# Performance work log

Measured on AMD Instinct MI355X. Metric: run time of the kernel, lower is better.

## Reference

```python
import jax, jax.numpy as jnp
import numpy as np

B, T, N = 128, 20, 49
VOCAB, EMB, HDIM, VDIM, ATT = 10000, 512, 1024, 512, 512
LN_EPS = 1e-5


def _layer_norm(x, g, b):
    mu = x.mean(-1, keepdims=True)
    var = ((x - mu) ** 2).mean(-1, keepdims=True)
    return (x - mu) * jax.lax.rsqrt(var + LN_EPS) * g + b


def _lstm_cell(x, h, c, Wih, Whh, bih, bhh):
    gates = x @ Wih.T + h @ Whh.T + bih + bhh  # [B, 4H]
    i, f, g, o = jnp.split(gates, 4, axis=-1)  # torch LSTMCell gate order
    c_new = jax.nn.sigmoid(f) * c + jax.nn.sigmoid(i) * jnp.tanh(g)
    h_new = jax.nn.sigmoid(o) * jnp.tanh(c_new)
    return h_new, c_new


def setup_inputs() -> dict:
    key = jax.random.key(0)
    ks = jax.random.split(key, 16)
    w = lambda k, shape: (jax.random.normal(k, shape, jnp.float32) * 0.02)
    embed_W = w(ks[2], (VOCAB, EMB)).at[0].set(0.0)  # padding_idx=0 row is zeros
    return dict(
        V=jax.random.normal(ks[0], (B, N, VDIM), jnp.float32),
        y=jax.random.randint(ks[1], (B, T), 0, VOCAB),
        embed_W=embed_W,
        Vp_W=w(ks[3], (HDIM, VDIM)), Vp_b=jnp.zeros((HDIM,), jnp.float32),
        attW=w(ks[4], (ATT, HDIM)), attU=w(ks[5], (ATT, HDIM)), attv=w(ks[6], (1, ATT)),
        l1_Wih=w(ks[7], (4 * HDIM, EMB + HDIM)), l1_Whh=w(ks[8], (4 * HDIM, HDIM)),
        l1_bih=jnp.zeros((4 * HDIM,), jnp.float32), l1_bhh=jnp.zeros((4 * HDIM,), jnp.float32),
        l2_Wih=w(ks[9], (4 * HDIM, HDIM)), l2_Whh=w(ks[10], (4 * HDIM, HDIM)),
        l2_bih=jnp.zeros((4 * HDIM,), jnp.float32), l2_bhh=jnp.zeros((4 * HDIM,), jnp.float32),
        n1_g=jnp.ones((HDIM,), jnp.float32), n1_b=jnp.zeros((HDIM,), jnp.float32),
        n2_g=jnp.ones((HDIM,), jnp.float32), n2_b=jnp.zeros((HDIM,), jnp.float32),
        ih_W=w(ks[11], (HDIM, HDIM)), ih_b=jnp.zeros((HDIM,), jnp.float32),
        ic_W=w(ks[12], (HDIM, HDIM)), ic_b=jnp.zeros((HDIM,), jnp.float32),
        proj_W=w(ks[13], (EMB, HDIM)),
    )


def reference(V, y, embed_W, Vp_W, Vp_b, attW, attU, attv,
              l1_Wih, l1_Whh, l1_bih, l1_bhh,
              l2_Wih, l2_Whh, l2_bih, l2_bhh,
              n1_g, n1_b, n2_g, n2_b,
              ih_W, ih_b, ic_W, ic_b, proj_W):
    Vp = V @ Vp_W.T + Vp_b                      # [B, N, H]
    feat_mean = Vp.mean(1)                      # [B, H]
    h1 = jnp.tanh(feat_mean @ ih_W.T + ih_b)
    c1 = jnp.tanh(feat_mean @ ic_W.T + ic_b)
    h2 = jnp.zeros_like(h1)
    c2 = jnp.zeros_like(c1)

    Uv = Vp @ attU.T                            # [B, N, ATT] (hoisted out of loop)
    emb_y = embed_W[y]                          # [B, T, EMB]
    xs = jnp.swapaxes(emb_y[:, :-1], 0, 1)      # [T-1, B, EMB]

    def step(carry, x_t):
        h1, c1, h2, c2 = carry
        # additive attention (dropout is identity in eval)
        e = jnp.tanh((h2 @ attW.T)[:, None, :] + Uv) @ attv[0]   # [B, N]
        a = jax.nn.softmax(e, axis=1)
        ctx = jnp.einsum('bn,bnh->bh', a, Vp)
        h1n, c1n = _lstm_cell(jnp.concatenate([x_t, ctx], -1), h1, c1,
                              l1_Wih, l1_Whh, l1_bih, l1_bhh)
        h1n = _layer_norm(h1n, n1_g, n1_b)
        h2n, c2n = _lstm_cell(h1n, h2, c2, l2_Wih, l2_Whh, l2_bih, l2_bhh)
        h2n = _layer_norm(h2n, n2_g, n2_b)
        logit = (h2n @ proj_W.T) @ embed_W.T    # [B, VOCAB]
        return (h1n, c1n, h2n, c2n), logit

    _, logits = jax.lax.scan(step, (h1, c1, h2, c2), xs)
    return jnp.swapaxes(logits, 0, 1)           # [B, T-1, VOCAB]
```

## Files before the change

### kernel.cpp

```cpp
#include <hip/hip_runtime.h>
#include <hip/hip_bf16.h>

#define TSTEPS 19

typedef short bf16x8 __attribute__((ext_vector_type(8)));
typedef short bf16x4 __attribute__((ext_vector_type(4)));
typedef float f32x4 __attribute__((ext_vector_type(4)));

__device__ __forceinline__ f32x4 mfma_bf16(bf16x8 a, bf16x8 b, f32x4 c) {
    return __builtin_amdgcn_mfma_f32_16x16x32_bf16(a, b, c, 0, 0, 0);
}
__device__ __forceinline__ short f2b(float f) {
    union { float f; unsigned u; } v; v.f = f;
    unsigned r = v.u + 0x7fffu + ((v.u >> 16) & 1u);
    return (short)(r >> 16);
}
__device__ __forceinline__ float b2f(short s) {
    union { unsigned u; float f; } v; v.u = ((unsigned)(unsigned short)s) << 16;
    return v.f;
}
__device__ __forceinline__ float sigm(float x) { return 1.f / (1.f + __expf(-x)); }
__device__ __forceinline__ float tanhfast(float x) { return 1.f - 2.f / (__expf(2.f * x) + 1.f); }

__global__ __launch_bounds__(256) void k_convert(
    const float* __restrict__ l1_Wih, const float* __restrict__ l1_Whh,
    const float* __restrict__ l2_Wih, const float* __restrict__ l2_Whh,
    const float* __restrict__ embed_W, const float* __restrict__ proj_W,
    const float* __restrict__ attW, const float* __restrict__ ih_W,
    const float* __restrict__ ic_W, const float* __restrict__ Vp_W,
    const float* __restrict__ attU, const float* __restrict__ V,
    const int* __restrict__ y, const float* __restrict__ n1g,
    const float* __restrict__ n2g,
    short* __restrict__ l1h, short* __restrict__ l1l,
    short* __restrict__ l2h, short* __restrict__ l2l,
    short* __restrict__ embB, short* __restrict__ pa, short* __restrict__ ihic,
    short* __restrict__ VpWh, short* __restrict__ VpWl, short* __restrict__ attUb,
    short* __restrict__ Vbh, short* __restrict__ Vbl, short* __restrict__ xall) {
    const int N1 = 4096 * 2560, N2 = 4096 * 2048, N3 = 10000 * 512, N4 = 1024 * 1024,
              N5 = 2048 * 1024, N6 = 1024 * 512, N7 = 512 * 1024, N8 = 128 * 49 * 512,
              N9 = 19 * 128 * 512;
    const int total4 = (N1 + N2 + N3 + N4 + N5 + N6 + N7 + N8 + N9) >> 2;
    int stride = gridDim.x * blockDim.x;
    for (int g = blockIdx.x * blockDim.x + threadIdx.x; g < total4; g += stride) {
        int e = g << 2;
        if (e < N1) {
            int n = e / 2560, k = e - n * 2560;
            f32x4 v;
            if (k < 1536) {
                v = *(const f32x4*)(l1_Wih + (size_t)n * 1536 + k);
            } else {
                f32x4 w = *(const f32x4*)(l1_Whh + (size_t)n * 1024 + (k - 1536));
                f32x4 gg = *(const f32x4*)(n1g + (k - 1536));
#pragma unroll
                for (int j = 0; j < 4; j++) v[j] = gg[j] * w[j];
            }
            bf16x4 hi, lo;
#pragma unroll
            for (int j = 0; j < 4; j++) { hi[j] = f2b(v[j]); lo[j] = f2b(v[j] - b2f(hi[j])); }
            *(bf16x4*)(l1h + e) = hi; *(bf16x4*)(l1l + e) = lo; continue;
        }
        e -= N1;
        if (e < N2) {
            int n = e >> 11, k = e & 2047;
            f32x4 w, gg;
            if (k < 1024) {
                w = *(const f32x4*)(l2_Wih + (size_t)n * 1024 + k);
                gg = *(const f32x4*)(n1g + k);
            } else {
                w = *(const f32x4*)(l2_Whh + (size_t)n * 1024 + (k - 1024));
                gg = *(const f32x4*)(n2g + (k - 1024));
            }
            bf16x4 hi, lo;
#pragma unroll
            for (int j = 0; j < 4; j++) {
                float v = gg[j] * w[j];
                hi[j] = f2b(v); lo[j] = f2b(v - b2f(hi[j]));
            }
            *(bf16x4*)(l2h + e) = hi; *(bf16x4*)(l2l + e) = lo; continue;
        }
        e -= N2;
        if (e < N3) {
            f32x4 v = *(const f32x4*)(embed_W + e);
            bf16x4 o;
#pragma unroll
            for (int j = 0; j < 4; j++) o[j] = f2b(v[j]);
            *(bf16x4*)(embB + e) = o; continue;
        }
        e -= N3;
        if (e < N4) {
            int n = e >> 10, k = e & 1023;
            f32x4 w = (n < 512) ? *(const f32x4*)(proj_W + (size_t)n * 1024 + k)
                                : *(const f32x4*)(attW + (size_t)(n - 512) * 1024 + k);
            f32x4 gg = *(const f32x4*)(n2g + k);
            bf16x4 o;
#pragma unroll
            for (int j = 0; j < 4; j++) o[j] = f2b(gg[j] * w[j]);
            *(bf16x4*)(pa + e) = o; continue;
        }
        e -= N4;
        if (e < N5) {
            int n = e >> 10, k = e & 1023;
            f32x4 w = (n < 1024) ? *(const f32x4*)(ih_W + (size_t)n * 1024 + k)
                                 : *(const f32x4*)(ic_W + (size_t)(n - 1024) * 1024 + k);
            bf16x4 o;
#pragma unroll
            for (int j = 0; j < 4; j++) o[j] = f2b(w[j]);
            *(bf16x4*)(ihic + e) = o; continue;
        }
        e -= N5;
        if (e < N6) {
            f32x4 v = *(const f32x4*)(Vp_W + e);
            bf16x4 hi, lo;
#pragma unroll
            for (int j = 0; j < 4; j++) { hi[j] = f2b(v[j]); lo[j] = f2b(v[j] - b2f(hi[j])); }
            *(bf16x4*)(VpWh + e) = hi; *(bf16x4*)(VpWl + e) = lo; continue;
        }
        e -= N6;
        if (e < N7) {
            f32x4 v = *(const f32x4*)(attU + e);
            bf16x4 o;
#pragma unroll
            for (int j = 0; j < 4; j++) o[j] = f2b(v[j]);
            *(bf16x4*)(attUb + e) = o; continue;
        }
        e -= N7;
        if (e < N8) {
            f32x4 v = *(const f32x4*)(V + e);
            bf16x4 hi, lo;
#pragma unroll
            for (int j = 0; j < 4; j++) { hi[j] = f2b(v[j]); lo[j] = f2b(v[j] - b2f(hi[j])); }
            *(bf16x4*)(Vbh + e) = hi; *(bf16x4*)(Vbl + e) = lo; continue;
        }
        e -= N8;
        {
            int t = e >> 16; int r = e & 65535;
            int b = r >> 9, k = r & 511;
            int idx = y[b * 20 + t];
            f32x4 v = *(const f32x4*)(embed_W + (size_t)idx * 512 + k);
            bf16x4 o;
#pragma unroll
            for (int j = 0; j < 4; j++) o[j] = f2b(v[j]);
            *(bf16x4*)(xall + e) = o;
        }
    }
}

__global__ __launch_bounds__(256) void k_corr(
    const float* __restrict__ l1_Whh, const float* __restrict__ l2_Wih,
    const float* __restrict__ l2_Whh, const float* __restrict__ proj_W,
    const float* __restrict__ attW,
    const float* __restrict__ n1g, const float* __restrict__ n1b,
    const float* __restrict__ n2g, const float* __restrict__ n2b,
    float* __restrict__ wg1, float* __restrict__ wb1,
    float* __restrict__ wg2a, float* __restrict__ wb2a,
    float* __restrict__ wg2b, float* __restrict__ wb2b,
    float* __restrict__ wgp, float* __restrict__ wbp) {
    int w = (blockIdx.x * 256 + threadIdx.x) >> 6;
    int lane = threadIdx.x & 63;
    if (w >= 13312) return;
    const float* row; const float* g; const float* b; float* og; float* ob;
    if (w < 4096)       { row = l1_Whh + (size_t)w * 1024; g = n1g; b = n1b; og = wg1 + w; ob = wb1 + w; }
    else if (w < 8192)  { int j = w - 4096; row = l2_Wih + (size_t)j * 1024; g = n1g; b = n1b; og = wg2a + j; ob = wb2a + j; }
    else if (w < 12288) { int j = w - 8192; row = l2_Whh + (size_t)j * 1024; g = n2g; b = n2b; og = wg2b + j; ob = wb2b + j; }
    else                { int j = w - 12288;
                          row = (j < 512) ? proj_W + (size_t)j * 1024 : attW + (size_t)(j - 512) * 1024;
                          g = n2g; b = n2b; og = wgp + j; ob = wbp + j; }
    float sg = 0.f, sb = 0.f;
    for (int k = lane; k < 1024; k += 64) { float wv = row[k]; sg += g[k] * wv; sb += b[k] * wv; }
#pragma unroll
    for (int o = 1; o < 64; o <<= 1) { sg += __shfl_xor(sg, o); sb += __shfl_xor(sb, o); }
    if (lane == 0) { *og = sg; *ob = sb; }
}

__device__ __forceinline__ void gemm_core(const short* __restrict__ A, int lda,
                                          const short* __restrict__ Bm, int ldb,
                                          int mb, int n0, int K, int Nlim,
                                          f32x4 acc[2][4]) {
    int lane = threadIdx.x & 63, wave = threadIdx.x >> 6;
    int col = lane & 15, quad = lane >> 4;
    const short* a0p = A + (size_t)(mb + wave * 32 + col) * lda + quad * 8;
    const short* a1p = a0p + (size_t)16 * lda;
    const short* bp[4];
#pragma unroll
    for (int s = 0; s < 4; s++) {
        int n = n0 + s * 16 + col;
        if (n >= Nlim) n = 0;
        bp[s] = Bm + (size_t)n * ldb + quad * 8;
    }
    for (int kb = 0; kb < K; kb += 32) {
        bf16x8 a0 = *(const bf16x8*)(a0p + kb);
        bf16x8 a1 = *(const bf16x8*)(a1p + kb);
#pragma unroll
        for (int s = 0; s < 4; s++) {
            bf16x8 b = *(const bf16x8*)(bp[s] + kb);
            acc[0][s] = mfma_bf16(a0, b, acc[0][s]);
            acc[1][s] = mfma_bf16(a1, b, acc[1][s]);
        }
    }
}

__global__ __launch_bounds__(256) void k_gemm_vp(const short* __restrict__ Ah,
                                                 const short* __restrict__ Al,
                                                 const short* __restrict__ Bh,
                                                 const short* __restrict__ Bl,
                                                 const float* __restrict__ Vp_b,
                                                 short* __restrict__ Vph,
                                                 short* __restrict__ Vpl) {
    int lane = threadIdx.x & 63, wave = threadIdx.x >> 6, col = lane & 15, quad = lane >> 4;
    int mb = blockIdx.y * 128, n0 = blockIdx.x * 64;
    f32x4 acc[2][4] = {};
    const short* ah0 = Ah + (size_t)(mb + wave * 32 + col) * 512 + quad * 8;
    const short* al0 = Al + (size_t)(mb + wave * 32 + col) * 512 + quad * 8;
    const short* ah1 = ah0 + 16 * 512; const short* al1 = al0 + 16 * 512;
    const short* bh[4]; const short* bl[4];
#pragma unroll
    for (int s = 0; s < 4; s++) {
        int n = n0 + s * 16 + col;
        bh[s] = Bh + (size_t)n * 512 + quad * 8; bl[s] = Bl + (size_t)n * 512 + quad * 8;
    }
    for (int kb = 0; kb < 512; kb += 32) {
        bf16x8 h0 = *(const bf16x8*)(ah0 + kb), l0 = *(const bf16x8*)(al0 + kb);
        bf16x8 h1 = *(const bf16x8*)(ah1 + kb), l1 = *(const bf16x8*)(al1 + kb);
#pragma unroll
        for (int s = 0; s < 4; s++) {
            bf16x8 wh = *(const bf16x8*)(bh[s] + kb);
            bf16x8 wl = *(const bf16x8*)(bl[s] + kb);
            acc[0][s] = mfma_bf16(h0, wh, acc[0][s]);
            acc[0][s] = mfma_bf16(l0, wh, acc[0][s]);
            acc[0][s] = mfma_bf16(h0, wl, acc[0][s]);
            acc[1][s] = mfma_bf16(h1, wh, acc[1][s]);
            acc[1][s] = mfma_bf16(l1, wh, acc[1][s]);
            acc[1][s] = mfma_bf16(h1, wl, acc[1][s]);
        }
    }
#pragma unroll
    for (int i = 0; i < 2; i++)
#pragma unroll
        for (int s = 0; s < 4; s++) {
            int n = n0 + s * 16 + col;
            float bias = Vp_b[n];
#pragma unroll
            for (int r = 0; r < 4; r++) {
                int m = mb + wave * 32 + i * 16 + quad * 4 + r;
                float v = acc[i][s][r] + bias;
                short hi = f2b(v);
                Vph[(size_t)m * 1024 + n] = hi;
                Vpl[(size_t)m * 1024 + n] = f2b(v - b2f(hi));
            }
        }
}

__global__ __launch_bounds__(256) void k_gemm_uv(const short* __restrict__ Vph,
                                                 const short* __restrict__ Vpl,
                                                 const short* __restrict__ attUb,
                                                 short* __restrict__ Uv) {
    int lane = threadIdx.x & 63, wave = threadIdx.x >> 6, col = lane & 15, quad = lane >> 4;
    int mb = blockIdx.y * 128, n0 = blockIdx.x * 64;
    f32x4 acc[2][4] = {};
    const short* ah0 = Vph + (size_t)(mb + wave * 32 + col) * 1024 + quad * 8;
    const short* al0 = Vpl + (size_t)(mb + wave * 32 + col) * 1024 + quad * 8;
    const short* ah1 = ah0 + 16 * 1024; const short* al1 = al0 + 16 * 1024;
    const short* bp[4];
#pragma unroll
    for (int s = 0; s < 4; s++) bp[s] = attUb + (size_t)(n0 + s * 16 + col) * 1024 + quad * 8;
    for (int kb = 0; kb < 1024; kb += 32) {
        bf16x8 h0 = *(const bf16x8*)(ah0 + kb), l0 = *(const bf16x8*)(al0 + kb);
        bf16x8 h1 = *(const bf16x8*)(ah1 + kb), l1 = *(const bf16x8*)(al1 + kb);
#pragma unroll
        for (int s = 0; s < 4; s++) {
            bf16x8 b = *(const bf16x8*)(bp[s] + kb);
            acc[0][s] = mfma_bf16(h0, b, acc[0][s]);
            acc[0][s] = mfma_bf16(l0, b, acc[0][s]);
            acc[1][s] = mfma_bf16(h1, b, acc[1][s]);
            acc[1][s] = mfma_bf16(l1, b, acc[1][s]);
        }
    }
#pragma unroll
    for (int i = 0; i < 2; i++)
#pragma unroll
        for (int s = 0; s < 4; s++) {
            int n = n0 + s * 16 + col;
#pragma unroll
            for (int r = 0; r < 4; r++) {
                int m = mb + wave * 32 + i * 16 + quad * 4 + r;
                Uv[(size_t)m * 512 + n] = f2b(acc[i][s][r]);
            }
        }
}

__global__ __launch_bounds__(256) void k_gemm_xpart(const short* __restrict__ xall,
                                                    const short* __restrict__ l1h,
                                                    float* __restrict__ xpart) {
    f32x4 acc[2][4] = {};
    int mb = blockIdx.y * 128, n0 = blockIdx.x * 64;
    gemm_core(xall, 512, l1h, 2560, mb, n0, 512, 1 << 30, acc);
    int lane = threadIdx.x & 63, wave = threadIdx.x >> 6, col = lane & 15, quad = lane >> 4;
#pragma unroll
    for (int i = 0; i < 2; i++)
#pragma unroll
        for (int s = 0; s < 4; s++) {
            int n = n0 + s * 16 + col;
#pragma unroll
            for (int r = 0; r < 4; r++) {
                int m = mb + wave * 32 + i * 16 + quad * 4 + r;
                xpart[(size_t)m * 4096 + n] = acc[i][s][r];
            }
        }
}

__global__ __launch_bounds__(256) void k_feat(const short* __restrict__ Vph,
                                              const short* __restrict__ Vpl,
                                              short* __restrict__ feat,
                                              float* __restrict__ c2,
                                              short* __restrict__ h2h1,
                                              short* __restrict__ h2l1,
                                              float* __restrict__ st1,
                                              float* __restrict__ st2) {
    int b = blockIdx.x, tid = threadIdx.x;
    int h0 = tid * 4;
    float acc[4] = {0.f, 0.f, 0.f, 0.f};
    for (int n = 0; n < 49; n++) {
        bf16x4 vh = *(const bf16x4*)(Vph + ((size_t)b * 49 + n) * 1024 + h0);
        bf16x4 vl = *(const bf16x4*)(Vpl + ((size_t)b * 49 + n) * 1024 + h0);
#pragma unroll
        for (int j = 0; j < 4; j++) acc[j] += b2f(vh[j]) + b2f(vl[j]);
    }
    bf16x4 o;
#pragma unroll
    for (int j = 0; j < 4; j++) o[j] = f2b(acc[j] * (1.f / 49.f));
    *(bf16x4*)(feat + (size_t)b * 1024 + h0) = o;
#pragma unroll
    for (int j = 0; j < 4; j++) {
        c2[(size_t)b * 1024 + h0 + j] = 0.f;
        h2h1[(size_t)b * 1024 + h0 + j] = 0;
        h2l1[(size_t)b * 1024 + h0 + j] = 0;
    }
    if (tid == 0) {
        st1[(128 + b) * 2] = 0.f; st1[(128 + b) * 2 + 1] = 1.f;
        st2[(128 + b) * 2] = 0.f; st2[(128 + b) * 2 + 1] = 1.f;
    }
}

__global__ __launch_bounds__(256) void k_gemm_h1c1(const short* __restrict__ feat,
                                                   const short* __restrict__ ihic,
                                                   const float* __restrict__ ih_b,
                                                   const float* __restrict__ ic_b,
                                                   short* __restrict__ h1h1,
                                                   short* __restrict__ h1l1,
                                                   float* __restrict__ c1) {
    f32x4 acc[2][4] = {};
    int n0 = blockIdx.y * 64;
    gemm_core(feat, 1024, ihic, 1024, 0, n0, 1024, 1 << 30, acc);
    int lane = threadIdx.x & 63, wave = threadIdx.x >> 6, col = lane & 15, quad = lane >> 4;
#pragma unroll
    for (int i = 0; i < 2; i++)
#pragma unroll
        for (int s = 0; s < 4; s++) {
            int n = n0 + s * 16 + col;
#pragma unroll
            for (int r = 0; r < 4; r++) {
                int m = wave * 32 + i * 16 + quad * 4 + r;
                float v = acc[i][s][r];
                if (n < 1024) {
                    float t = tanhfast(v + ih_b[n]);
                    short hi = f2b(t);
                    h1h1[(size_t)m * 1024 + n] = hi;
                    h1l1[(size_t)m * 1024 + n] = f2b(t - b2f(hi));
                } else {
                    c1[(size_t)m * 1024 + (n - 1024)] = tanhfast(v + ic_b[n - 1024]);
                }
            }
        }
}

__global__ __launch_bounds__(256) void k_attn(
        int t,
        const float* __restrict__ pproj,
        const float* __restrict__ st2p,
        const float* __restrict__ wgp, const float* __restrict__ wbp,
        short* __restrict__ pbuf_prev,
        const short* __restrict__ Uv,
        const float* __restrict__ attv, const short* __restrict__ Vph,
        const short* __restrict__ Vpl,
        short* __restrict__ ctxh, short* __restrict__ ctxl) {
    int b = blockIdx.x, tid = threadIdx.x;
    int lane = tid & 63, wave = tid >> 6;
    __shared__ float shW[512];
    __shared__ float se[49], sa[49];
    if (t == 0) {
        shW[tid] = 0.f; shW[tid + 256] = 0.f;
    } else {
        float mu = st2p[b * 2], rs = st2p[b * 2 + 1];
        int n4 = tid * 4;
        f32x4 p0 = *(const f32x4*)(pproj + (size_t)b * 1024 + n4);
        f32x4 p1 = *(const f32x4*)(pproj + 131072 + (size_t)b * 1024 + n4);
        f32x4 wb = *(const f32x4*)(wbp + n4);
        f32x4 wg = *(const f32x4*)(wgp + n4);
        float v[4];
#pragma unroll
        for (int j = 0; j < 4; j++) v[j] = rs * (p0[j] + p1[j]) + wb[j] - rs * mu * wg[j];
        if (n4 < 512) {
            bf16x4 o;
#pragma unroll
            for (int j = 0; j < 4; j++) o[j] = f2b(v[j]);
            *(bf16x4*)(pbuf_prev + (size_t)b * 512 + n4) = o;
        } else {
#pragma unroll
            for (int j = 0; j < 4; j++) shW[n4 - 512 + j] = v[j];
        }
    }
    __syncthreads();
    for (int n = wave; n < 49; n += 4) {
        const float* hw = shW + lane * 8;
        const short* uv = Uv + ((size_t)b * 49 + n) * 512 + lane * 8;
        const float* av = attv + lane * 8;
        bf16x8 u8 = *(const bf16x8*)uv;
        float part = 0.f;
#pragma unroll
        for (int j = 0; j < 8; j++) part += tanhfast(hw[j] + b2f(u8[j])) * av[j];
#pragma unroll
        for (int o = 1; o < 64; o <<= 1) part += __shfl_xor(part, o);
        if (lane == 0) se[n] = part;
    }
    __syncthreads();
    if (wave == 0) {
        float v = (lane < 49) ? se[lane] : -1e30f;
        float mx = v;
#pragma unroll
        for (int o = 1; o < 64; o <<= 1) mx = fmaxf(mx, __shfl_xor(mx, o));
        float p = (lane < 49) ? __expf(v - mx) : 0.f;
        float s = p;
#pragma unroll
        for (int o = 1; o < 64; o <<= 1) s += __shfl_xor(s, o);
        if (lane < 49) sa[lane] = p / s;
    }
    __syncthreads();
    {
        int h0 = tid * 4;
        float acc[4] = {0.f, 0.f, 0.f, 0.f};
        for (int n = 0; n < 49; n++) {
            float wgt = sa[n];
            bf16x4 vh = *(const bf16x4*)(Vph + ((size_t)b * 49 + n) * 1024 + h0);
            bf16x4 vl = *(const bf16x4*)(Vpl + ((size_t)b * 49 + n) * 1024 + h0);
#pragma unroll
            for (int j = 0; j < 4; j++) acc[j] += wgt * (b2f(vh[j]) + b2f(vl[j]));
        }
        bf16x4 oh, ol;
#pragma unroll
        for (int j = 0; j < 4; j++) {
            short hi = f2b(acc[j]); oh[j] = hi; ol[j] = f2b(acc[j] - b2f(hi));
        }
        *(bf16x4*)(ctxh + (size_t)b * 1024 + h0) = oh;
        *(bf16x4*)(ctxl + (size_t)b * 1024 + h0) = ol;
    }
}

__global__ __launch_bounds__(256) void k_lstm1_mm(
        const short* __restrict__ ctxh, const short* __restrict__ ctxl,
        const short* __restrict__ h1hp, const short* __restrict__ h1lp,
        const short* __restrict__ l1h, const short* __restrict__ l1l,
        float* __restrict__ part) {
    int bn = blockIdx.x, bk = blockIdx.y;
    int lane = threadIdx.x & 63, wave = threadIdx.x >> 6, col = lane & 15, quad = lane >> 4;
    int n0 = bn * 64;
    int kw0 = 512 + bk * 512;
    f32x4 acc[2][4] = {};
    const short* bh[4]; const short* bl[4];
#pragma unroll
    for (int s = 0; s < 4; s++) {
        size_t o = (size_t)(n0 + s * 16 + col) * 2560 + kw0 + quad * 8;
        bh[s] = l1h + o; bl[s] = l1l + o;
    }
    int r0 = wave * 32 + col;
    const short* Ah = (bk < 2) ? ctxh : h1hp;
    const short* Al = (bk < 2) ? ctxl : h1lp;
    int ko = (bk & 1) * 512;
    const short* a0h = Ah + (size_t)r0 * 1024 + ko + quad * 8;
    const short* a0l = Al + (size_t)r0 * 1024 + ko + quad * 8;
    const short* a1h = a0h + 16 * 1024; const short* a1l = a0l + 16 * 1024;
    for (int kb = 0; kb < 512; kb += 32) {
        bf16x8 h0 = *(const bf16x8*)(a0h + kb), l0 = *(const bf16x8*)(a0l + kb);
        bf16x8 h1 = *(const bf16x8*)(a1h + kb), l1 = *(const bf16x8*)(a1l + kb);
#pragma unroll
        for (int s = 0; s < 4; s++) {
            bf16x8 wh = *(const bf16x8*)(bh[s] + kb);
            bf16x8 wl = *(const bf16x8*)(bl[s] + kb);
            acc[0][s] = mfma_bf16(h0, wh, acc[0][s]);
            acc[0][s] = mfma_bf16(l0, wh, acc[0][s]);
            acc[0][s] = mfma_bf16(h0, wl, acc[0][s]);
            acc[1][s] = mfma_bf16(h1, wh, acc[1][s]);
            acc[1][s] = mfma_bf16(l1, wh, acc[1][s]);
            acc[1][s] = mfma_bf16(h1, wl, acc[1][s]);
        }
    }
#pragma unroll
    for (int i = 0; i < 2; i++)
#pragma unroll
        for (int s = 0; s < 4; s++)
#pragma unroll
            for (int r = 0; r < 4; r++) {
                int m = wave * 32 + i * 16 + quad * 4 + r;
                part[((size_t)bk * 128 + m) * 4096 + n0 + s * 16 + col] = acc[i][s][r];
            }
}

__global__ __launch_bounds__(256) void k_red1(const float* __restrict__ part,
        const float* __restrict__ xpart_t,
        const float* __restrict__ st_prev,
        const float* __restrict__ wg1, const float* __restrict__ wb1,
        const float* __restrict__ bih, const float* __restrict__ bhh,
        float* __restrict__ c1, short* __restrict__ h1hc, short* __restrict__ h1lc,
        float* __restrict__ st_cur) {
    int m = blockIdx.x, tid = threadIdx.x;
    float mu_p = st_prev[m * 2], rs_p = st_prev[m * 2 + 1];
    const size_t SB = 128UL * 4096;
    int h = tid * 4;
    float pre[4][4];
#pragma unroll
    for (int g = 0; g < 4; g++) {
        int n = g * 1024 + h;
        size_t base = (size_t)m * 4096 + n;
        f32x4 pX = *(const f32x4*)(xpart_t + base);
        f32x4 p0 = *(const f32x4*)(part + base);
        f32x4 p1 = *(const f32x4*)(part + SB + base);
        f32x4 p2 = *(const f32x4*)(part + 2 * SB + base);
        f32x4 p3 = *(const f32x4*)(part + 3 * SB + base);
        f32x4 wb = *(const f32x4*)(wb1 + n);
        f32x4 wg = *(const f32x4*)(wg1 + n);
        f32x4 bi = *(const f32x4*)(bih + n);
        f32x4 bh = *(const f32x4*)(bhh + n);
#pragma unroll
        for (int j = 0; j < 4; j++)
            pre[g][j] = (pX[j] + p0[j] + p1[j]) + rs_p * (p2[j] + p3[j])
                        + wb[j] - rs_p * mu_p * wg[j] + bi[j] + bh[j];
    }
    size_t idx = (size_t)m * 1024 + h;
    f32x4 cv = *(const f32x4*)(c1 + idx);
    f32x4 cn_v; bf16x4 oh, ol;
    float s1 = 0.f, s2 = 0.f;
#pragma unroll
    for (int j = 0; j < 4; j++) {
        float cn = sigm(pre[1][j]) * cv[j] + sigm(pre[0][j]) * tanhfast(pre[2][j]);
        float hn = sigm(pre[3][j]) * tanhfast(cn);
        cn_v[j] = cn;
        short hi = f2b(hn); oh[j] = hi; ol[j] = f2b(hn - b2f(hi));
        s1 += hn; s2 += hn * hn;
    }
    *(f32x4*)(c1 + idx) = cn_v;
    *(bf16x4*)(h1hc + idx) = oh;
    *(bf16x4*)(h1lc + idx) = ol;
    __shared__ float red[8];
    int lane = tid & 63, wave = tid >> 6;
#pragma unroll
    for (int o = 1; o < 64; o <<= 1) { s1 += __shfl_xor(s1, o); s2 += __shfl_xor(s2, o); }
    if (lane == 0) { red[wave * 2] = s1; red[wave * 2 + 1] = s2; }
    __syncthreads();
    if (tid == 0) {
        float S1 = red[0] + red[2] + red[4] + red[6];
        float S2 = red[1] + red[3] + red[5] + red[7];
        float mu = S1 * (1.f / 1024.f);
        float var = S2 * (1.f / 1024.f) - mu * mu;
        st_cur[m * 2] = mu; st_cur[m * 2 + 1] = rsqrtf(var + 1e-5f);
    }
}

__global__ __launch_bounds__(256) void k_lstm2_mm(
        const short* __restrict__ h1hc, const short* __restrict__ h1lc,
        const short* __restrict__ h2hp, const short* __restrict__ h2lp,
        const short* __restrict__ l2h, const short* __restrict__ l2l,
        float* __restrict__ part) {
    int bn = blockIdx.x, bk = blockIdx.y;
    int lane = threadIdx.x & 63, wave = threadIdx.x >> 6, col = lane & 15, quad = lane >> 4;
    int n0 = bn * 64;
    int kw0 = bk * 512;
    f32x4 acc[2][4] = {};
    const short* bh[4]; const short* bl[4];
#pragma unroll
    for (int s = 0; s < 4; s++) {
        size_t o = (size_t)(n0 + s * 16 + col) * 2048 + kw0 + quad * 8;
        bh[s] = l2h + o; bl[s] = l2l + o;
    }
    int r0 = wave * 32 + col;
    const short* Ah = (bk < 2) ? h1hc : h2hp;
    const short* Al = (bk < 2) ? h1lc : h2lp;
    int ko = (bk & 1) * 512;
    const short* a0h = Ah + (size_t)r0 * 1024 + ko + quad * 8;
    const short* a0l = Al + (size_t)r0 * 1024 + ko + quad * 8;
    const short* a1h = a0h + 16 * 1024; const short* a1l = a0l + 16 * 1024;
    for (int kb = 0; kb < 512; kb += 32) {
        bf16x8 h0 = *(const bf16x8*)(a0h + kb), l0 = *(const bf16x8*)(a0l + kb);
        bf16x8 h1 = *(const bf16x8*)(a1h + kb), l1 = *(const bf16x8*)(a1l + kb);
#pragma unroll
        for (int s = 0; s < 4; s++) {
            bf16x8 wh = *(const bf16x8*)(bh[s] + kb);
            bf16x8 wl = *(const bf16x8*)(bl[s] + kb);
            acc[0][s] = mfma_bf16(h0, wh, acc[0][s]);
            acc[0][s] = mfma_bf16(l0, wh, acc[0][s]);
            acc[0][s] = mfma_bf16(h0, wl, acc[0][s]);
            acc[1][s] = mfma_bf16(h1, wh, acc[1][s]);
            acc[1][s] = mfma_bf16(l1, wh, acc[1][s]);
            acc[1][s] = mfma_bf16(h1, wl, acc[1][s]);
        }
    }
#pragma unroll
    for (int i = 0; i < 2; i++)
#pragma unroll
        for (int s = 0; s < 4; s++)
#pragma unroll
            for (int r = 0; r < 4; r++) {
                int m = wave * 32 + i * 16 + quad * 4 + r;
                part[((size_t)bk * 128 + m) * 4096 + n0 + s * 16 + col] = acc[i][s][r];
            }
}

__global__ __launch_bounds__(256) void k_red2(const float* __restrict__ part,
        const float* __restrict__ stA, const float* __restrict__ stB,
        const float* __restrict__ wg2a, const float* __restrict__ wb2a,
        const float* __restrict__ wg2b, const float* __restrict__ wb2b,
        const float* __restrict__ bih, const float* __restrict__ bhh,
        float* __restrict__ c2, short* __restrict__ h2hc, short* __restrict__ h2lc,
        float* __restrict__ st_cur) {
    int m = blockIdx.x, tid = threadIdx.x;
    float mu1 = stA[m * 2], rs1 = stA[m * 2 + 1];
    float mu2 = stB[m * 2], rs2 = stB[m * 2 + 1];
    const size_t SB = 128UL * 4096;
    int h = tid * 4;
    float pre[4][4];
#pragma unroll
    for (int g = 0; g < 4; g++) {
        int n = g * 1024 + h;
        size_t base = (size_t)m * 4096 + n;
        f32x4 p0 = *(const f32x4*)(part + base);
        f32x4 p1 = *(const f32x4*)(part + SB + base);
        f32x4 p2 = *(const f32x4*)(part + 2 * SB + base);
        f32x4 p3 = *(const f32x4*)(part + 3 * SB + base);
        f32x4 wba = *(const f32x4*)(wb2a + n);
        f32x4 wga = *(const f32x4*)(wg2a + n);
        f32x4 wbb = *(const f32x4*)(wb2b + n);
        f32x4 wgb = *(const f32x4*)(wg2b + n);
        f32x4 bi = *(const f32x4*)(bih + n);
        f32x4 bh = *(const f32x4*)(bhh + n);
#pragma unroll
        for (int j = 0; j < 4; j++)
            pre[g][j] = rs1 * (p0[j] + p1[j]) + rs2 * (p2[j] + p3[j])
                        + wba[j] - rs1 * mu1 * wga[j]
                        + wbb[j] - rs2 * mu2 * wgb[j] + bi[j] + bh[j];
    }
    size_t idx = (size_t)m * 1024 + h;
    f32x4 cv = *(const f32x4*)(c2 + idx);
    f32x4 cn_v; bf16x4 oh, ol;
    float s1 = 0.f, s2 = 0.f;
#pragma unroll
    for (int j = 0; j < 4; j++) {
        float cn = sigm(pre[1][j]) * cv[j] + sigm(pre[0][j]) * tanhfast(pre[2][j]);
        float hn = sigm(pre[3][j]) * tanhfast(cn);
        cn_v[j] = cn;
        short hi = f2b(hn); oh[j] = hi; ol[j] = f2b(hn - b2f(hi));
        s1 += hn; s2 += hn * hn;
    }
    *(f32x4*)(c2 + idx) = cn_v;
    *(bf16x4*)(h2hc + idx) = oh;
    *(bf16x4*)(h2lc + idx) = ol;
    __shared__ float red[8];
    int lane = tid & 63, wave = tid >> 6;
#pragma unroll
    for (int o = 1; o < 64; o <<= 1) { s1 += __shfl_xor(s1, o); s2 += __shfl_xor(s2, o); }
    if (lane == 0) { red[wave * 2] = s1; red[wave * 2 + 1] = s2; }
    __syncthreads();
    if (tid == 0) {
        float S1 = red[0] + red[2] + red[4] + red[6];
        float S2 = red[1] + red[3] + red[5] + red[7];
        float mu = S1 * (1.f / 1024.f);
        float var = S2 * (1.f / 1024.f) - mu * mu;
        st_cur[m * 2] = mu; st_cur[m * 2 + 1] = rsqrtf(var + 1e-5f);
    }
}

__global__ __launch_bounds__(256) void k_projatt(
        const short* __restrict__ h2hc, const short* __restrict__ h2lc,
        const short* __restrict__ pa,
        float* __restrict__ pproj) {
    int nt = blockIdx.x, mh = blockIdx.y, kc = blockIdx.z;
    int tid = threadIdx.x, lane = tid & 63, wave = tid >> 6, col = lane & 15, quad = lane >> 4;
    int arow = mh * 64 + wave * 16 + col;
    int n = nt * 16 + col;
    int k0 = kc * 512;
    f32x4 acc = {};
    const short* bp = pa + (size_t)n * 1024 + k0 + quad * 8;
    const short* ah = h2hc + (size_t)arow * 1024 + k0 + quad * 8;
    const short* al = h2lc + (size_t)arow * 1024 + k0 + quad * 8;
    for (int kb = 0; kb < 512; kb += 32) {
        bf16x8 xh = *(const bf16x8*)(ah + kb);
        bf16x8 xl = *(const bf16x8*)(al + kb);
        bf16x8 b = *(const bf16x8*)(bp + kb);
        acc = mfma_bf16(xh, b, acc);
        acc = mfma_bf16(xl, b, acc);
    }
#pragma unroll
    for (int r = 0; r < 4; r++) {
        int m = mh * 64 + wave * 16 + quad * 4 + r;
        pproj[(size_t)kc * 131072 + (size_t)m * 1024 + nt * 16 + col] = acc[r];
    }
}

__global__ __launch_bounds__(256) void k_pbuf(const float* __restrict__ pproj,
        const float* __restrict__ st2c,
        const float* __restrict__ wgp, const float* __restrict__ wbp,
        short* __restrict__ pbuf) {
    int b = blockIdx.x, tid = threadIdx.x;
    float mu = st2c[b * 2], rs = st2c[b * 2 + 1];
#pragma unroll
    for (int j = 0; j < 2; j++) {
        int n = tid * 2 + j;
        float v = rs * (pproj[(size_t)b * 1024 + n] + pproj[131072 + (size_t)b * 1024 + n])
                  + wbp[n] - rs * mu * wgp[n];
        pbuf[(size_t)b * 512 + n] = f2b(v);
    }
}

__global__ __launch_bounds__(256) void k_logits_all(const short* __restrict__ pbuf_all,
                                                    const short* __restrict__ embB,
                                                    float* __restrict__ out) {
    int n0 = blockIdx.x * 64, t = blockIdx.y;
    __shared__ alignas(16) short Bs[64 * 512];
    char* Bsb = (char*)Bs;
    int tid = threadIdx.x, lane = tid & 63, wave = tid >> 6;
#pragma unroll
    for (int i = 0; i < 16; i++) {
        int r = i * 4 + wave;
        int n = n0 + r; if (n >= 10000) n = 0;
        bf16x8 v = *(const bf16x8*)(embB + (size_t)n * 512 + lane * 8);
        *(bf16x8*)(Bsb + r * 1024 + ((lane * 16) ^ ((r & 7) << 4))) = v;
    }
    __syncthreads();
    int col = lane & 15, quad = lane >> 4;
    f32x4 acc[2][4] = {};
    const short* A = pbuf_all + (size_t)t * 128 * 512;
    const short* a0p = A + (size_t)(wave * 32 + col) * 512 + quad * 8;
    const short* a1p = a0p + 16 * 512;
    int rbase[4], rkey[4];
#pragma unroll
    for (int s = 0; s < 4; s++) {
        int r = s * 16 + col;
        rbase[s] = r * 1024;
        rkey[s] = (r & 7) << 4;
    }
#pragma unroll 4
    for (int kb = 0; kb < 512; kb += 32) {
        bf16x8 a0 = *(const bf16x8*)(a0p + kb);
        bf16x8 a1 = *(const bf16x8*)(a1p + kb);
#pragma unroll
        for (int s = 0; s < 4; s++) {
            bf16x8 bfrag = *(const bf16x8*)(Bsb + rbase[s] + ((quad * 16 + kb * 2) ^ rkey[s]));
            acc[0][s] = mfma_bf16(a0, bfrag, acc[0][s]);
            acc[1][s] = mfma_bf16(a1, bfrag, acc[1][s]);
        }
    }
#pragma unroll
    for (int i = 0; i < 2; i++)
#pragma unroll
        for (int s = 0; s < 4; s++) {
            int n = n0 + s * 16 + col;
            if (n >= 10000) continue;
#pragma unroll
            for (int r = 0; r < 4; r++) {
                int m = wave * 32 + i * 16 + quad * 4 + r;
                out[((size_t)m * 19 + t) * 10000 + n] = acc[i][s][r];
            }
        }
}

extern "C" void kernel_launch(void* const* d_in, const int* in_sizes, int n_in,
                              void* d_out, int out_size, void* d_ws, size_t ws_size,
                              hipStream_t stream) {
    const float* V = (const float*)d_in[0];
    const int* y = (const int*)d_in[1];
    const float* embed_W = (const float*)d_in[2];
    const float* Vp_W = (const float*)d_in[3];
    const float* Vp_b = (const float*)d_in[4];
    const float* attW = (const float*)d_in[5];
    const float* attU = (const float*)d_in[6];
    const float* attv = (const float*)d_in[7];
    const float* l1_Wih = (const float*)d_in[8];
    const float* l1_Whh = (const float*)d_in[9];
    const float* l1_bih = (const float*)d_in[10];
    const float* l1_bhh = (const float*)d_in[11];
    const float* l2_Wih = (const float*)d_in[12];
    const float* l2_Whh = (const float*)d_in[13];
    const float* l2_bih = (const float*)d_in[14];
    const float* l2_bhh = (const float*)d_in[15];
    const float* n1g = (const float*)d_in[16];
    const float* n1b = (const float*)d_in[17];
    const float* n2g = (const float*)d_in[18];
    const float* n2b = (const float*)d_in[19];
    const float* ih_W = (const float*)d_in[20];
    const float* ih_b = (const float*)d_in[21];
    const float* ic_W = (const float*)d_in[22];
    const float* ic_b = (const float*)d_in[23];
    const float* proj_W = (const float*)d_in[24];
    float* out = (float*)d_out;
    (void)in_sizes; (void)n_in; (void)out_size;

    char* wsp = (char*)d_ws;
    size_t off = 0;
    auto alloc = [&](size_t bytes) -> void* {
        void* p = wsp + off;
        off += (bytes + 255) & ~(size_t)255;
        return p;
    };
    short* l1h  = (short*)alloc(4096UL * 2560 * 2);
    short* l1l  = (short*)alloc(4096UL * 2560 * 2);
    short* l2h  = (short*)alloc(4096UL * 2048 * 2);
    short* l2l  = (short*)alloc(4096UL * 2048 * 2);
    short* embB = (short*)alloc(10000UL * 512 * 2);
    short* pa   = (short*)alloc(1024UL * 1024 * 2);
    short* ihic = (short*)alloc(2048UL * 1024 * 2);
    short* VpWh = (short*)alloc(1024UL * 512 * 2);
    short* VpWl = (short*)alloc(1024UL * 512 * 2);
    short* attUb= (short*)alloc(512UL * 1024 * 2);
    short* Vbh  = (short*)alloc(128UL * 49 * 512 * 2);
    short* Vbl  = (short*)alloc(128UL * 49 * 512 * 2);
    short* xall = (short*)alloc(19UL * 128 * 512 * 2);
    short* Vph  = (short*)alloc(6272UL * 1024 * 2);
    short* Vpl  = (short*)alloc(6272UL * 1024 * 2);
    short* Uv   = (short*)alloc(6272UL * 512 * 2);
    short* feat = (short*)alloc(128UL * 1024 * 2);
    short* ctxh = (short*)alloc(128UL * 1024 * 2);
    short* ctxl = (short*)alloc(128UL * 1024 * 2);
    short* h1h  = (short*)alloc(2UL * 128 * 1024 * 2);
    short* h1l  = (short*)alloc(2UL * 128 * 1024 * 2);
    short* h2h  = (short*)alloc(2UL * 128 * 1024 * 2);
    short* h2l  = (short*)alloc(2UL * 128 * 1024 * 2);
    short* pbuf_all = (short*)alloc(19UL * 128 * 512 * 2);
    float* c1   = (float*)alloc(128UL * 1024 * 4);
    float* c2   = (float*)alloc(128UL * 1024 * 4);
    float* st1  = (float*)alloc(2UL * 128 * 2 * 4);
    float* st2  = (float*)alloc(2UL * 128 * 2 * 4);
    float* pmm1 = (float*)alloc(4UL * 128 * 4096 * 4);
    float* pmm2 = (float*)alloc(4UL * 128 * 4096 * 4);
    float* pproj= (float*)alloc(2UL * 128 * 1024 * 4);
    float* xpart= (float*)alloc(2432UL * 4096 * 4);
    float* wg1  = (float*)alloc(4096UL * 4);
    float* wb1  = (float*)alloc(4096UL * 4);
    float* wg2a = (float*)alloc(4096UL * 4);
    float* wb2a = (float*)alloc(4096UL * 4);
    float* wg2b = (float*)alloc(4096UL * 4);
    float* wb2b = (float*)alloc(4096UL * 4);
    float* wgp  = (float*)alloc(1024UL * 4);
    float* wbp  = (float*)alloc(1024UL * 4);
    if (off > ws_size) return;

    const size_t HB = 128UL * 1024;
    const size_t SB2 = 128UL * 2;

    k_convert<<<2048, 256, 0, stream>>>(l1_Wih, l1_Whh, l2_Wih, l2_Whh, embed_W, proj_W,
                                        attW, ih_W, ic_W, Vp_W, attU, V, y, n1g, n2g,
                                        l1h, l1l, l2h, l2l, embB, pa, ihic,
                                        VpWh, VpWl, attUb, Vbh, Vbl, xall);
    k_corr<<<3328, 256, 0, stream>>>(l1_Whh, l2_Wih, l2_Whh, proj_W, attW,
                                     n1g, n1b, n2g, n2b,
                                     wg1, wb1, wg2a, wb2a, wg2b, wb2b, wgp, wbp);
    k_gemm_vp<<<dim3(16, 49), 256, 0, stream>>>(Vbh, Vbl, VpWh, VpWl, Vp_b, Vph, Vpl);
    k_gemm_xpart<<<dim3(64, 19), 256, 0, stream>>>(xall, l1h, xpart);
    k_feat<<<128, 256, 0, stream>>>(Vph, Vpl, feat, c2, h2h + HB, h2l + HB, st1, st2);
    k_gemm_h1c1<<<dim3(1, 32), 256, 0, stream>>>(feat, ihic, ih_b, ic_b,
                                                 h1h + HB, h1l + HB, c1);
    k_gemm_uv<<<dim3(8, 49), 256, 0, stream>>>(Vph, Vpl, attUb, Uv);

    for (int t = 0; t < TSTEPS; t++) {
        int cur = t & 1, prev = cur ^ 1;
        short* pbuf_prev = pbuf_all + (size_t)(t > 0 ? t - 1 : 0) * 128 * 512;
        k_attn<<<128, 256, 0, stream>>>(t, pproj, st2 + prev * SB2, wgp, wbp,
                                        pbuf_prev, Uv, attv, Vph, Vpl, ctxh, ctxl);
        k_lstm1_mm<<<dim3(64, 4), 256, 0, stream>>>(ctxh, ctxl,
                                                    h1h + prev * HB, h1l + prev * HB,
                                                    l1h, l1l, pmm1);
        k_red1<<<128, 256, 0, stream>>>(pmm1, xpart + (size_t)t * 128 * 4096,
                                        st1 + prev * SB2, wg1, wb1,
                                        l1_bih, l1_bhh, c1,
                                        h1h + cur * HB, h1l + cur * HB, st1 + cur * SB2);
        k_lstm2_mm<<<dim3(64, 4), 256, 0, stream>>>(h1h + cur * HB, h1l + cur * HB,
                                                    h2h + prev * HB, h2l + prev * HB,
                                                    l2h, l2l, pmm2);
        k_red2<<<128, 256, 0, stream>>>(pmm2, st1 + cur * SB2, st2 + prev * SB2,
                                        wg2a, wb2a, wg2b, wb2b, l2_bih, l2_bhh, c2,
                                        h2h + cur * HB, h2l + cur * HB, st2 + cur * SB2);
        k_projatt<<<dim3(64, 2, 2), 256, 0, stream>>>(h2h + cur * HB, h2l + cur * HB,
                                                      pa, pproj);
    }
    k_pbuf<<<128, 256, 0, stream>>>(pproj, st2, wgp, wbp,
                                    pbuf_all + 18UL * 128 * 512);
    k_logits_all<<<dim3(157, 19), 256, 0, stream>>>(pbuf_all, embB, out);
}
```

Before: 2.332 ms.

## Stage weight tiles in swizzled LDS and double split-K for LSTM GEMMs

The Vp, Uv and both per-step LSTM GEMM kernels now copy each block's weight tile into shared memory once, using an XOR swizzle. Previously every wave read the shared B operand straight from global memory. The LSTM matmuls split K eight ways instead of four, giving 512 blocks per launch for more parallelism, and the reduce kernels sum eight partial buffers. The two partial buffers are merged into one. In exchange there are extra syncs, 64KB of LDS per block that limits occupancy, and more partial-sum traffic in the reductions.

```diff
diff --git a/kernel.cpp b/kernel.cpp
--- a/kernel.cpp
+++ b/kernel.cpp
@@ -206,31 +206,46 @@
                                                  const float* __restrict__ Vp_b,
                                                  short* __restrict__ Vph,
                                                  short* __restrict__ Vpl) {
-    int lane = threadIdx.x & 63, wave = threadIdx.x >> 6, col = lane & 15, quad = lane >> 4;
+    __shared__ alignas(16) short Bs[2 * 64 * 256];
+    char* Bsb = (char*)Bs;
+    int tid = threadIdx.x, lane = tid & 63, wave = tid >> 6, col = lane & 15, quad = lane >> 4;
     int mb = blockIdx.y * 128, n0 = blockIdx.x * 64;
     f32x4 acc[2][4] = {};
     const short* ah0 = Ah + (size_t)(mb + wave * 32 + col) * 512 + quad * 8;
     const short* al0 = Al + (size_t)(mb + wave * 32 + col) * 512 + quad * 8;
     const short* ah1 = ah0 + 16 * 512; const short* al1 = al0 + 16 * 512;
-    const short* bh[4]; const short* bl[4];
-#pragma unroll
-    for (int s = 0; s < 4; s++) {
-        int n = n0 + s * 16 + col;
-        bh[s] = Bh + (size_t)n * 512 + quad * 8; bl[s] = Bl + (size_t)n * 512 + quad * 8;
-    }
-    for (int kb = 0; kb < 512; kb += 32) {
-        bf16x8 h0 = *(const bf16x8*)(ah0 + kb), l0 = *(const bf16x8*)(al0 + kb);
-        bf16x8 h1 = *(const bf16x8*)(ah1 + kb), l1 = *(const bf16x8*)(al1 + kb);
-#pragma unroll
-        for (int s = 0; s < 4; s++) {
-            bf16x8 wh = *(const bf16x8*)(bh[s] + kb);
-            bf16x8 wl = *(const bf16x8*)(bl[s] + kb);
-            acc[0][s] = mfma_bf16(h0, wh, acc[0][s]);
-            acc[0][s] = mfma_bf16(l0, wh, acc[0][s]);
-            acc[0][s] = mfma_bf16(h0, wl, acc[0][s]);
-            acc[1][s] = mfma_bf16(h1, wh, acc[1][s]);
-            acc[1][s] = mfma_bf16(l1, wh, acc[1][s]);
-            acc[1][s] = mfma_bf16(h1, wl, acc[1][s]);
+#pragma unroll
+    for (int ph = 0; ph < 2; ph++) {
+        int kbase = ph * 256;
+        __syncthreads();
+#pragma unroll
+        for (int i = 0; i < 8; i++) {
+            int r = i * 8 + wave * 2 + (lane >> 5);
+            int n = n0 + r;
+            int e = (lane & 31) * 8;
+            bf16x8 vh = *(const bf16x8*)(Bh + (size_t)n * 512 + kbase + e);
+            bf16x8 vl = *(const bf16x8*)(Bl + (size_t)n * 512 + kbase + e);
+            int wo = r * 512 + ((e * 2) ^ ((r & 7) << 4));
+            *(bf16x8*)(Bsb + wo) = vh;
+            *(bf16x8*)(Bsb + 32768 + wo) = vl;
+        }
+        __syncthreads();
+        for (int kb = 0; kb < 256; kb += 32) {
+            bf16x8 h0 = *(const bf16x8*)(ah0 + kbase + kb), l0 = *(const bf16x8*)(al0 + kbase + kb);
+            bf16x8 h1 = *(const bf16x8*)(ah1 + kbase + kb), l1 = *(const bf16x8*)(al1 + kbase + kb);
+#pragma unroll
+            for (int s = 0; s < 4; s++) {
+                int r = s * 16 + col;
+                int off = r * 512 + ((quad * 16 + kb * 2) ^ ((r & 7) << 4));
+                bf16x8 wh = *(const bf16x8*)(Bsb + off);
+                bf16x8 wl = *(const bf16x8*)(Bsb + 32768 + off);
+                acc[0][s] = mfma_bf16(h0, wh, acc[0][s]);
+                acc[0][s] = mfma_bf16(l0, wh, acc[0][s]);
+                acc[0][s] = mfma_bf16(h0, wl, acc[0][s]);
+                acc[1][s] = mfma_bf16(h1, wh, acc[1][s]);
+                acc[1][s] = mfma_bf16(l1, wh, acc[1][s]);
+                acc[1][s] = mfma_bf16(h1, wl, acc[1][s]);
+            }
         }
     }
 #pragma unroll
@@ -254,25 +269,39 @@
                                                  const short* __restrict__ Vpl,
                                                  const short* __restrict__ attUb,
                                                  short* __restrict__ Uv) {
-    int lane = threadIdx.x & 63, wave = threadIdx.x >> 6, col = lane & 15, quad = lane >> 4;
+    __shared__ alignas(16) short Bs[64 * 512];
+    char* Bsb = (char*)Bs;
+    int tid = threadIdx.x, lane = tid & 63, wave = tid >> 6, col = lane & 15, quad = lane >> 4;
     int mb = blockIdx.y * 128, n0 = blockIdx.x * 64;
     f32x4 acc[2][4] = {};
     const short* ah0 = Vph + (size_t)(mb + wave * 32 + col) * 1024 + quad * 8;
     const short* al0 = Vpl + (size_t)(mb + wave * 32 + col) * 1024 + quad * 8;
     const short* ah1 = ah0 + 16 * 1024; const short* al1 = al0 + 16 * 1024;
-    const short* bp[4];
-#pragma unroll
-    for (int s = 0; s < 4; s++) bp[s] = attUb + (size_t)(n0 + s * 16 + col) * 1024 + quad * 8;
-    for (int kb = 0; kb < 1024; kb += 32) {
-        bf16x8 h0 = *(const bf16x8*)(ah0 + kb), l0 = *(const bf16x8*)(al0 + kb);
-        bf16x8 h1 = *(const bf16x8*)(ah1 + kb), l1 = *(const bf16x8*)(al1 + kb);
-#pragma unroll
-        for (int s = 0; s < 4; s++) {
-            bf16x8 b = *(const bf16x8*)(bp[s] + kb);
-            acc[0][s] = mfma_bf16(h0, b, acc[0][s]);
-            acc[0][s] = mfma_bf16(l0, b, acc[0][s]);
-            acc[1][s] = mfma_bf16(h1, b, acc[1][s]);
-            acc[1][s] = mfma_bf16(l1, b, acc[1][s]);
+#pragma unroll
+    for (int ph = 0; ph < 2; ph++) {
+        int kbase = ph * 512;
+        __syncthreads();
+#pragma unroll
+        for (int i = 0; i < 16; i++) {
+            int r = i * 4 + wave;
+            int n = n0 + r;
+            int e = lane * 8;
+            bf16x8 v = *(const bf16x8*)(attUb + (size_t)n * 1024 + kbase + e);
+            *(bf16x8*)(Bsb + r * 1024 + ((e * 2) ^ ((r & 7) << 4))) = v;
+        }
+        __syncthreads();
+        for (int kb = 0; kb < 512; kb += 32) {
+            bf16x8 h0 = *(const bf16x8*)(ah0 + kbase + kb), l0 = *(const bf16x8*)(al0 + kbase + kb);
+            bf16x8 h1 = *(const bf16x8*)(ah1 + kbase + kb), l1 = *(const bf16x8*)(al1 + kbase + kb);
+#pragma unroll
+            for (int s = 0; s < 4; s++) {
+                int r = s * 16 + col;
+                bf16x8 b = *(const bf16x8*)(Bsb + r * 1024 + ((quad * 16 + kb * 2) ^ ((r & 7) << 4)));
+                acc[0][s] = mfma_bf16(h0, b, acc[0][s]);
+                acc[0][s] = mfma_bf16(l0, b, acc[0][s]);
+                acc[1][s] = mfma_bf16(h1, b, acc[1][s]);
+                acc[1][s] = mfma_bf16(l1, b, acc[1][s]);
+            }
         }
     }
 #pragma unroll
@@ -460,31 +489,41 @@
         const short* __restrict__ h1hp, const short* __restrict__ h1lp,
         const short* __restrict__ l1h, const short* __restrict__ l1l,
         float* __restrict__ part) {
+    __shared__ alignas(16) short Bs[2 * 64 * 256];
+    char* Bsb = (char*)Bs;
     int bn = blockIdx.x, bk = blockIdx.y;
-    int lane = threadIdx.x & 63, wave = threadIdx.x >> 6, col = lane & 15, quad = lane >> 4;
+    int tid = threadIdx.x, lane = tid & 63, wave = tid >> 6, col = lane & 15, quad = lane >> 4;
     int n0 = bn * 64;
-    int kw0 = 512 + bk * 512;
+    int kw0 = 512 + bk * 256;
+#pragma unroll
+    for (int i = 0; i < 8; i++) {
+        int r = i * 8 + wave * 2 + (lane >> 5);
+        int e = (lane & 31) * 8;
+        size_t src = (size_t)(n0 + r) * 2560 + kw0 + e;
+        bf16x8 vh = *(const bf16x8*)(l1h + src);
+        bf16x8 vl = *(const bf16x8*)(l1l + src);
+        int wo = r * 512 + ((e * 2) ^ ((r & 7) << 4));
+        *(bf16x8*)(Bsb + wo) = vh;
+        *(bf16x8*)(Bsb + 32768 + wo) = vl;
+    }
+    __syncthreads();
     f32x4 acc[2][4] = {};
-    const short* bh[4]; const short* bl[4];
-#pragma unroll
-    for (int s = 0; s < 4; s++) {
-        size_t o = (size_t)(n0 + s * 16 + col) * 2560 + kw0 + quad * 8;
-        bh[s] = l1h + o; bl[s] = l1l + o;
-    }
     int r0 = wave * 32 + col;
-    const short* Ah = (bk < 2) ? ctxh : h1hp;
-    const short* Al = (bk < 2) ? ctxl : h1lp;
-    int ko = (bk & 1) * 512;
+    const short* Ah = (bk < 4) ? ctxh : h1hp;
+    const short* Al = (bk < 4) ? ctxl : h1lp;
+    int ko = (bk & 3) * 256;
     const short* a0h = Ah + (size_t)r0 * 1024 + ko + quad * 8;
     const short* a0l = Al + (size_t)r0 * 1024 + ko + quad * 8;
     const short* a1h = a0h + 16 * 1024; const short* a1l = a0l + 16 * 1024;
-    for (int kb = 0; kb < 512; kb += 32) {
+    for (int kb = 0; kb < 256; kb += 32) {
         bf16x8 h0 = *(const bf16x8*)(a0h + kb), l0 = *(const bf16x8*)(a0l + kb);
         bf16x8 h1 = *(const bf16x8*)(a1h + kb), l1 = *(const bf16x8*)(a1l + kb);
 #pragma unroll
         for (int s = 0; s < 4; s++) {
-            bf16x8 wh = *(const bf16x8*)(bh[s] + kb);
-            bf16x8 wl = *(const bf16x8*)(bl[s] + kb);
+            int r = s * 16 + col;
+            int off = r * 512 + ((quad * 16 + kb * 2) ^ ((r & 7) << 4));
+            bf16x8 wh = *(const bf16x8*)(Bsb + off);
+            bf16x8 wl = *(const bf16x8*)(Bsb + 32768 + off);
             acc[0][s] = mfma_bf16(h0, wh, acc[0][s]);
             acc[0][s] = mfma_bf16(l0, wh, acc[0][s]);
             acc[0][s] = mfma_bf16(h0, wl, acc[0][s]);
@@ -520,19 +559,22 @@
     for (int g = 0; g < 4; g++) {
         int n = g * 1024 + h;
         size_t base = (size_t)m * 4096 + n;
-        f32x4 pX = *(const f32x4*)(xpart_t + base);
-        f32x4 p0 = *(const f32x4*)(part + base);
-        f32x4 p1 = *(const f32x4*)(part + SB + base);
-        f32x4 p2 = *(const f32x4*)(part + 2 * SB + base);
-        f32x4 p3 = *(const f32x4*)(part + 3 * SB + base);
+        f32x4 pA = *(const f32x4*)(xpart_t + base);
+        f32x4 pB = {};
+#pragma unroll
+        for (int q = 0; q < 4; q++) {
+            f32x4 pa_ = *(const f32x4*)(part + q * SB + base);
+            f32x4 pb_ = *(const f32x4*)(part + (q + 4) * SB + base);
+#pragma unroll
+            for (int j = 0; j < 4; j++) { pA[j] += pa_[j]; pB[j] += pb_[j]; }
+        }
         f32x4 wb = *(const f32x4*)(wb1 + n);
         f32x4 wg = *(const f32x4*)(wg1 + n);
         f32x4 bi = *(const f32x4*)(bih + n);
         f32x4 bh = *(const f32x4*)(bhh + n);
 #pragma unroll
         for (int j = 0; j < 4; j++)
-            pre[g][j] = (pX[j] + p0[j] + p1[j]) + rs_p * (p2[j] + p3[j])
-                        + wb[j] - rs_p * mu_p * wg[j] + bi[j] + bh[j];
+            pre[g][j] = pA[j] + rs_p * pB[j] + wb[j] - rs_p * mu_p * wg[j] + bi[j] + bh[j];
     }
     size_t idx = (size_t)m * 1024 + h;
     f32x4 cv = *(const f32x4*)(c1 + idx);
@@ -569,31 +611,41 @@
         const short* __restrict__ h2hp, const short* __restrict__ h2lp,
         const short* __restrict__ l2h, const short* __restrict__ l2l,
         float* __restrict__ part) {
+    __shared__ alignas(16) short Bs[2 * 64 * 256];
+    char* Bsb = (char*)Bs;
     int bn = blockIdx.x, bk = blockIdx.y;
-    int lane = threadIdx.x & 63, wave = threadIdx.x >> 6, col = lane & 15, quad = lane >> 4;
+    int tid = threadIdx.x, lane = tid & 63, wave = tid >> 6, col = lane & 15, quad = lane >> 4;
     int n0 = bn * 64;
-    int kw0 = bk * 512;
+    int kw0 = bk * 256;
+#pragma unroll
+    for (int i = 0; i < 8; i++) {
+        int r = i * 8 + wave * 2 + (lane >> 5);
+        int e = (lane & 31) * 8;
+        size_t src = (size_t)(n0 + r) * 2048 + kw0 + e;
+        bf16x8 vh = *(const bf16x8*)(l2h + src);
+        bf16x8 vl = *(const bf16x8*)(l2l + src);
+        int wo = r * 512 + ((e * 2) ^ ((r & 7) << 4));
+        *(bf16x8*)(Bsb + wo) = vh;
+        *(bf16x8*)(Bsb + 32768 + wo) = vl;
+    }
+    __syncthreads();
     f32x4 acc[2][4] = {};
-    const short* bh[4]; const short* bl[4];
-#pragma unroll
-    for (int s = 0; s < 4; s++) {
-        size_t o = (size_t)(n0 + s * 16 + col) * 2048 + kw0 + quad * 8;
-        bh[s] = l2h + o; bl[s] = l2l + o;
-    }
     int r0 = wave * 32 + col;
-    const short* Ah = (bk < 2) ? h1hc : h2hp;
-    const short* Al = (bk < 2) ? h1lc : h2lp;
-    int ko = (bk & 1) * 512;
+    const short* Ah = (bk < 4) ? h1hc : h2hp;
+    const short* Al = (bk < 4) ? h1lc : h2lp;
+    int ko = (bk & 3) * 256;
     const short* a0h = Ah + (size_t)r0 * 1024 + ko + quad * 8;
     const short* a0l = Al + (size_t)r0 * 1024 + ko + quad * 8;
     const short* a1h = a0h + 16 * 1024; const short* a1l = a0l + 16 * 1024;
-    for (int kb = 0; kb < 512; kb += 32) {
+    for (int kb = 0; kb < 256; kb += 32) {
         bf16x8 h0 = *(const bf16x8*)(a0h + kb), l0 = *(const bf16x8*)(a0l + kb);
         bf16x8 h1 = *(const bf16x8*)(a1h + kb), l1 = *(const bf16x8*)(a1l + kb);
 #pragma unroll
         for (int s = 0; s < 4; s++) {
-            bf16x8 wh = *(const bf16x8*)(bh[s] + kb);
-            bf16x8 wl = *(const bf16x8*)(bl[s] + kb);
+            int r = s * 16 + col;
+            int off = r * 512 + ((quad * 16 + kb * 2) ^ ((r & 7) << 4));
+            bf16x8 wh = *(const bf16x8*)(Bsb + off);
+            bf16x8 wl = *(const bf16x8*)(Bsb + 32768 + off);
             acc[0][s] = mfma_bf16(h0, wh, acc[0][s]);
             acc[0][s] = mfma_bf16(l0, wh, acc[0][s]);
             acc[0][s] = mfma_bf16(h0, wl, acc[0][s]);
@@ -630,10 +682,14 @@
     for (int g = 0; g < 4; g++) {
         int n = g * 1024 + h;
         size_t base = (size_t)m * 4096 + n;
-        f32x4 p0 = *(const f32x4*)(part + base);
-        f32x4 p1 = *(const f32x4*)(part + SB + base);
-        f32x4 p2 = *(const f32x4*)(part + 2 * SB + base);
-        f32x4 p3 = *(const f32x4*)(part + 3 * SB + base);
+        f32x4 pA = {}, pB = {};
+#pragma unroll
+        for (int q = 0; q < 4; q++) {
+            f32x4 pa_ = *(const f32x4*)(part + q * SB + base);
+            f32x4 pb_ = *(const f32x4*)(part + (q + 4) * SB + base);
+#pragma unroll
+            for (int j = 0; j < 4; j++) { pA[j] += pa_[j]; pB[j] += pb_[j]; }
+        }
         f32x4 wba = *(const f32x4*)(wb2a + n);
         f32x4 wga = *(const f32x4*)(wg2a + n);
         f32x4 wbb = *(const f32x4*)(wb2b + n);
@@ -642,7 +698,7 @@
         f32x4 bh = *(const f32x4*)(bhh + n);
 #pragma unroll
         for (int j = 0; j < 4; j++)
-            pre[g][j] = rs1 * (p0[j] + p1[j]) + rs2 * (p2[j] + p3[j])
+            pre[g][j] = rs1 * pA[j] + rs2 * pB[j]
                         + wba[j] - rs1 * mu1 * wga[j]
                         + wbb[j] - rs2 * mu2 * wgb[j] + bi[j] + bh[j];
     }
@@ -836,8 +892,7 @@
     float* c2   = (float*)alloc(128UL * 1024 * 4);
     float* st1  = (float*)alloc(2UL * 128 * 2 * 4);
     float* st2  = (float*)alloc(2UL * 128 * 2 * 4);
-    float* pmm1 = (float*)alloc(4UL * 128 * 4096 * 4);
-    float* pmm2 = (float*)alloc(4UL * 128 * 4096 * 4);
+    float* pmm  = (float*)alloc(8UL * 128 * 4096 * 4);
     float* pproj= (float*)alloc(2UL * 128 * 1024 * 4);
     float* xpart= (float*)alloc(2432UL * 4096 * 4);
     float* wg1  = (float*)alloc(4096UL * 4);
@@ -872,17 +927,17 @@
         short* pbuf_prev = pbuf_all + (size_t)(t > 0 ? t - 1 : 0) * 128 * 512;
         k_attn<<<128, 256, 0, stream>>>(t, pproj, st2 + prev * SB2, wgp, wbp,
                                         pbuf_prev, Uv, attv, Vph, Vpl, ctxh, ctxl);
-        k_lstm1_mm<<<dim3(64, 4), 256, 0, stream>>>(ctxh, ctxl,
+        k_lstm1_mm<<<dim3(64, 8), 256, 0, stream>>>(ctxh, ctxl,
                                                     h1h + prev * HB, h1l + prev * HB,
-                                                    l1h, l1l, pmm1);
-        k_red1<<<128, 256, 0, stream>>>(pmm1, xpart + (size_t)t * 128 * 4096,
+                                                    l1h, l1l, pmm);
+        k_red1<<<128, 256, 0, stream>>>(pmm, xpart + (size_t)t * 128 * 4096,
                                         st1 + prev * SB2, wg1, wb1,
                                         l1_bih, l1_bhh, c1,
                                         h1h + cur * HB, h1l + cur * HB, st1 + cur * SB2);
-        k_lstm2_mm<<<dim3(64, 4), 256, 0, stream>>>(h1h + cur * HB, h1l + cur * HB,
+        k_lstm2_mm<<<dim3(64, 8), 256, 0, stream>>>(h1h + cur * HB, h1l + cur * HB,
                                                     h2h + prev * HB, h2l + prev * HB,
-                                                    l2h, l2l, pmm2);
-        k_red2<<<128, 256, 0, stream>>>(pmm2, st1 + cur * SB2, st2 + prev * SB2,
+                                                    l2h, l2l, pmm);
+        k_red2<<<128, 256, 0, stream>>>(pmm, st1 + cur * SB2, st2 + prev * SB2,
                                         wg2a, wb2a, wg2b, wb2b, l2_bih, l2_bhh, c2,
                                         h2h + cur * HB, h2l + cur * HB, st2 + cur * SB2);
         k_projatt<<<dim3(64, 2, 2), 256, 0, stream>>>(h2h + cur * HB, h2l + cur * HB,
```

New measurement: 1.958 ms. 1.19x faster.
